# Optimization experiments

Measured on AMD Instinct MI355X. Metric: run time of the kernel, lower is better.

Reference implementation:

```python
import jax, jax.numpy as jnp
import numpy as np

K_V_DIM = 100
_SQRT_D = float(np.sqrt(K_V_DIM))


def _dk_layer(q, k, v, Wq, bq, Wk, n_unsqueeze):
    """One DKEncoder_layer: DK_text + DK_knowledge + DK_fusion (CokeBert attention).
    q: [B, q_dim]; k: [..., n, K_V_DIM]; v: [..., n, d_v].
    Attention over the last neighbor axis n.
    """
    # DK_text: linear + tanh + unsqueeze to broadcast against k
    q_i = jnp.tanh(q @ Wq.T + bq)                               # [B, D]
    q_i = q_i.reshape((q_i.shape[0],) + (1,) * n_unsqueeze + (K_V_DIM,))
    # DK_knowledge: bias-free linear on k
    k = k @ Wk.T
    # DK_fusion (CokeBert): scaled dot, mask zeros, leaky_relu+softmax, zero out fully-masked rows
    attn = (q_i * k).sum(-1) / _SQRT_D                          # [..., n]
    attn = jnp.where(attn == 0.0, -10000.0, attn)
    attn = jax.nn.softmax(jax.nn.leaky_relu(attn), axis=-1)
    n = attn.shape[-1]
    attn = jnp.where(attn == 1.0 / n, 0.0, attn)
    return jnp.einsum('...n,...nd->...d', attn, v)              # [..., d_v]


def setup_inputs() -> dict:
    key = jax.random.key(0)
    ks = jax.random.split(key, 12)
    B, S, E, N1, N2, D, Q = 8, 256, 256, 16, 16, K_V_DIM, 768
    return {
        "input_ent": jax.random.randint(ks[0], (B, S), 0, 2, dtype=jnp.int64),
        "q": jax.random.normal(ks[1], (B, S, Q), dtype=jnp.float32),
        "k1": jax.random.normal(ks[2], (B, E, N1, D), dtype=jnp.float32),
        "v1": jax.random.normal(ks[3], (B, E, N1, D), dtype=jnp.float32),
        "k2": jax.random.normal(ks[4], (B, E, N1, N2, D), dtype=jnp.float32),
        "v2": jax.random.normal(ks[5], (B, E, N1, N2, D), dtype=jnp.float32),
        # layers[0] has layer_no=2 (deepest), layers[1] has layer_no=1
        "Wq2": jax.random.normal(ks[6], (D, Q), dtype=jnp.float32) * 0.05,
        "bq2": jnp.zeros((D,), dtype=jnp.float32),
        "Wk2": jax.random.normal(ks[7], (D, D), dtype=jnp.float32) * 0.1,
        "Wq1": jax.random.normal(ks[8], (D, Q), dtype=jnp.float32) * 0.05,
        "bq1": jnp.zeros((D,), dtype=jnp.float32),
        "Wk1": jax.random.normal(ks[9], (D, D), dtype=jnp.float32) * 0.1,
    }


def reference(input_ent, q, k1, v1, k2, v2, Wq2, bq2, Wk2, Wq1, bq1, Wk1):
    q0 = q[:, 0, :]                                             # [B, Q]
    # layer 0 (layer_no=2): reduce innermost neighbor axis
    combined = _dk_layer(q0, k2, v2, Wq2, bq2, Wk2, 3)          # [B, E, N1, D]
    # layer 1 (layer_no=1): v = cat([v1, combined])
    v1c = jnp.concatenate([v1, combined], axis=-1)              # [B, E, N1, 2D]
    combined = _dk_layer(q0, k1, v1c, Wq1, bq1, Wk1, 2)         # [B, E, 2D]
    # scatter: i-th nonzero position of input_ent[b] receives combined[b, i]
    mask = input_ent != 0                                       # [B, S]
    rank = jnp.cumsum(mask.astype(jnp.int32), axis=1) - 1       # [B, S]
    rank = jnp.clip(rank, 0, combined.shape[1] - 1)
    gathered = jnp.take_along_axis(combined, rank[..., None], axis=1)  # [B, S, 2D]
    return jnp.where(mask[..., None], gathered, 0.0)
```

## Files before the change

### kernel.cpp

```cpp
#include <hip/hip_runtime.h>
#include <cstddef>
#include <cstdint>

#define BB 8
#define SS 256
#define EE 256
#define NN1 16
#define NN2 16
#define DD 100
#define QQ 768

__device__ __forceinline__ float dot4(float4 a, float4 b) {
    return a.x * b.x + a.y * b.y + a.z * b.z + a.w * b.w;
}

__global__ __launch_bounds__(256) void prep_kernel(
    const float* __restrict__ q, const int* __restrict__ ent,
    const float* __restrict__ Wq2, const float* __restrict__ bq2, const float* __restrict__ Wk2,
    const float* __restrict__ Wq1, const float* __restrict__ bq1, const float* __restrict__ Wk1,
    float* __restrict__ qk2o, float* __restrict__ qk1o, int* __restrict__ rk)
{
    const int blk = blockIdx.x, t = threadIdx.x;
    if (blk < 16) {
        const int b = blk >> 1, layer = blk & 1;
        const float* Wq = layer ? Wq1 : Wq2;
        const float* bq = layer ? bq1 : bq2;
        const float* Wk = layer ? Wk1 : Wk2;
        float* qko      = layer ? qk1o : qk2o;
        __shared__ float s_q[QQ];
        __shared__ float s_qi[DD];
        for (int i = t; i < QQ; i += 256) s_q[i] = q[(size_t)b * SS * QQ + i];
        __syncthreads();
        const float4* sq4 = (const float4*)s_q;
        const int r = t & 7;
        for (int d = t >> 3; d < DD; d += 32) {
            const float4* wq4 = (const float4*)(Wq + (size_t)d * QQ);
            float acc = 0.f;
            for (int c = r; c < QQ / 4; c += 8) acc += dot4(wq4[c], sq4[c]);
            acc += __shfl_xor(acc, 1, 8);
            acc += __shfl_xor(acc, 2, 8);
            acc += __shfl_xor(acc, 4, 8);
            if (r == 0) s_qi[d] = tanhf(acc + bq[d]);
        }
        __syncthreads();
        if (t < DD) {
            float acc = 0.f;
            for (int d = 0; d < DD; ++d) acc += s_qi[d] * Wk[d * DD + t];
            qko[b * DD + t] = 0.1f * acc;
        }
    } else {
        const int b = blk - 16;
        __shared__ int s_m[SS];
        const int m = (ent[b * SS + t] != 0) ? 1 : 0;
        s_m[t] = m;
        __syncthreads();
        for (int off = 1; off < SS; off <<= 1) {
            const int add = (t >= off) ? s_m[t - off] : 0;
            __syncthreads();
            s_m[t] += add;
            __syncthreads();
        }
        int rank = s_m[t] - 1;
        rank = rank < 0 ? 0 : (rank > EE - 1 ? EE - 1 : rank);
        rk[b * SS + t] = m ? rank : -1;
    }
}

__global__ __launch_bounds__(64) void dk2_kernel(
    const float* __restrict__ k2, const float* __restrict__ v2,
    const float* __restrict__ qk2g, float* __restrict__ c2o,
    int b0, int nunits)
{
    const int t = threadIdx.x;
    __shared__ float4 s_pp[400];
    float* s_part = (float*)s_pp;

    int u = blockIdx.x;
    const int stride = gridDim.x;
    const size_t gofs = (size_t)b0 * 4096;

    float4 ka[7];
    if (u < nunits) {
        const float4* kt = (const float4*)k2 + (gofs + u) * 400;
        #pragma unroll
        for (int j = 0; j < 6; ++j) ka[j] = kt[t + 64 * j];
        if (t < 16) ka[6] = kt[384 + t];
    }

    while (u < nunits) {
        const int b = b0 + (u >> 12);
        const float4* qk = (const float4*)qk2g + b * 25;
        const float4* vt = (const float4*)v2 + (gofs + u) * 400;

        float4 va[7];
        #pragma unroll
        for (int j = 0; j < 6; ++j) va[j] = vt[t + 64 * j];
        if (t < 16) va[6] = vt[384 + t];

        #pragma unroll
        for (int j = 0; j < 6; ++j) {
            const int i = t + 64 * j;
            s_part[i] = dot4(ka[j], qk[i % 25]);
        }
        if (t < 16) { const int i = 384 + t; s_part[i] = dot4(ka[6], qk[i % 25]); }

        const int un = u + stride;
        if (un < nunits) {
            const float4* ktn = (const float4*)k2 + (gofs + un) * 400;
            #pragma unroll
            for (int j = 0; j < 6; ++j) ka[j] = ktn[t + 64 * j];
            if (t < 16) ka[6] = ktn[384 + t];
        }

        __syncthreads();
        float p = 0.f;
        {
            float lg = 0.f;
            if (t < 16) {
                #pragma unroll
                for (int c = 0; c < 25; ++c) lg += s_part[t * 25 + c];
                if (lg == 0.0f) lg = -10000.0f;
                lg = lg >= 0.f ? lg : 0.01f * lg;
            }
            float mx = lg;
            mx = fmaxf(mx, __shfl_xor(mx, 1, 16));
            mx = fmaxf(mx, __shfl_xor(mx, 2, 16));
            mx = fmaxf(mx, __shfl_xor(mx, 4, 16));
            mx = fmaxf(mx, __shfl_xor(mx, 8, 16));
            const float e = __expf(lg - mx);
            float sm = e;
            sm += __shfl_xor(sm, 1, 16);
            sm += __shfl_xor(sm, 2, 16);
            sm += __shfl_xor(sm, 4, 16);
            sm += __shfl_xor(sm, 8, 16);
            p = e / sm;
            if (p == 0.0625f) p = 0.f;
        }
        __syncthreads();

        #pragma unroll
        for (int j = 0; j < 6; ++j) {
            const int i = t + 64 * j;
            const float pn = __shfl(p, i / 25, 64);
            s_pp[i] = make_float4(pn * va[j].x, pn * va[j].y, pn * va[j].z, pn * va[j].w);
        }
        if (t < 16) {
            const int i = 384 + t;
            const float pn = __shfl(p, 15, 64);
            s_pp[i] = make_float4(pn * va[6].x, pn * va[6].y, pn * va[6].z, pn * va[6].w);
        }
        __syncthreads();

        if (t < 25) {
            float4 a = make_float4(0.f, 0.f, 0.f, 0.f);
            #pragma unroll
            for (int n = 0; n < 16; ++n) {
                const float4 x = s_pp[n * 25 + t];
                a.x += x.x; a.y += x.y; a.z += x.z; a.w += x.w;
            }
            ((float4*)c2o)[(size_t)u * 25 + t] = a;
        }
        __syncthreads();
        u = un;
    }
}

__global__ __launch_bounds__(64) void dk1_kernel(
    const float* __restrict__ k1, const float* __restrict__ v1,
    const float* __restrict__ c2i, const float* __restrict__ qk1g,
    float* __restrict__ comb, int b0)
{
    const int blk  = blockIdx.x;
    const int bbe  = blk >> 1;
    const int half = blk & 1;
    const int b    = b0 + (bbe >> 8);
    const int be   = (b << 8) | (bbe & 255);
    const int t    = threadIdx.x;

    __shared__ float4 s_pp[400];
    float* s_part = (float*)s_pp;

    const float4* kt = (const float4*)k1 + (size_t)be * 400;
    const float4* vt = half ? (const float4*)c2i + (size_t)bbe * 400
                            : (const float4*)v1 + (size_t)be * 400;
    const float4* qk = (const float4*)qk1g + b * 25;

    float4 ka[7], va[7];
    #pragma unroll
    for (int j = 0; j < 6; ++j) { ka[j] = kt[t + 64 * j]; va[j] = vt[t + 64 * j]; }
    if (t < 16) { ka[6] = kt[384 + t]; va[6] = vt[384 + t]; }

    #pragma unroll
    for (int j = 0; j < 6; ++j) {
        const int i = t + 64 * j;
        s_part[i] = dot4(ka[j], qk[i % 25]);
    }
    if (t < 16) { const int i = 384 + t; s_part[i] = dot4(ka[6], qk[i % 25]); }
    __syncthreads();

    float p = 0.f;
    {
        float lg = 0.f;
        if (t < 16) {
            #pragma unroll
            for (int c = 0; c < 25; ++c) lg += s_part[t * 25 + c];
            if (lg == 0.0f) lg = -10000.0f;
            lg = lg >= 0.f ? lg : 0.01f * lg;
        }
        float mx = lg;
        mx = fmaxf(mx, __shfl_xor(mx, 1, 16));
        mx = fmaxf(mx, __shfl_xor(mx, 2, 16));
        mx = fmaxf(mx, __shfl_xor(mx, 4, 16));
        mx = fmaxf(mx, __shfl_xor(mx, 8, 16));
        const float e = __expf(lg - mx);
        float sm = e;
        sm += __shfl_xor(sm, 1, 16);
        sm += __shfl_xor(sm, 2, 16);
        sm += __shfl_xor(sm, 4, 16);
        sm += __shfl_xor(sm, 8, 16);
        p = e / sm;
        if (p == 0.0625f) p = 0.f;
    }
    __syncthreads();

    #pragma unroll
    for (int j = 0; j < 6; ++j) {
        const int i = t + 64 * j;
        const float pn = __shfl(p, i / 25, 64);
        s_pp[i] = make_float4(pn * va[j].x, pn * va[j].y, pn * va[j].z, pn * va[j].w);
    }
    if (t < 16) {
        const int i = 384 + t;
        const float pn = __shfl(p, 15, 64);
        s_pp[i] = make_float4(pn * va[6].x, pn * va[6].y, pn * va[6].z, pn * va[6].w);
    }
    __syncthreads();

    if (t < 25) {
        float4 a = make_float4(0.f, 0.f, 0.f, 0.f);
        #pragma unroll
        for (int n = 0; n < 16; ++n) {
            const float4 x = s_pp[n * 25 + t];
            a.x += x.x; a.y += x.y; a.z += x.z; a.w += x.w;
        }
        ((float4*)comb)[(size_t)be * 50 + half * 25 + t] = a;
    }
}

__global__ __launch_bounds__(64) void gather_kernel(
    const float* __restrict__ comb, const int* __restrict__ rk, float* __restrict__ out)
{
    const int bs = blockIdx.x;
    const int b  = bs >> 8;
    const int t  = threadIdx.x;
    const int r  = rk[bs];
    float* o = out + (size_t)bs * (2 * DD);
    if (r < 0) {
        for (int d = t; d < 2 * DD; d += 64) o[d] = 0.f;
    } else {
        const float* src = comb + (size_t)(b * EE + r) * (2 * DD);
        for (int d = t; d < 2 * DD; d += 64) o[d] = src[d];
    }
}

extern "C" void kernel_launch(void* const* d_in, const int* in_sizes, int n_in,
                              void* d_out, int out_size, void* d_ws, size_t ws_size,
                              hipStream_t stream)
{
    const int*   ent = (const int*)d_in[0];
    const float* q   = (const float*)d_in[1];
    const float* k1  = (const float*)d_in[2];
    const float* v1  = (const float*)d_in[3];
    const float* k2  = (const float*)d_in[4];
    const float* v2  = (const float*)d_in[5];
    const float* Wq2 = (const float*)d_in[6];
    const float* bq2 = (const float*)d_in[7];
    const float* Wk2 = (const float*)d_in[8];
    const float* Wq1 = (const float*)d_in[9];
    const float* bq1 = (const float*)d_in[10];
    const float* Wk1 = (const float*)d_in[11];
    float* out = (float*)d_out;

    float* ws   = (float*)d_ws;
    float* qk2  = ws;
    float* qk1  = ws + 1024;
    int*   rk   = (int*)(ws + 2048);
    float* comb = ws + 4096;
    float* c2   = ws + 4096 + 409600;

    const size_t fixed = 4096 + 409600;
    const size_t perb  = (size_t)EE * NN1 * DD;
    size_t wsf = ws_size / sizeof(float);
    int kb = (wsf > fixed) ? (int)((wsf - fixed) / perb) : 1;
    if (kb < 1) kb = 1;
    if (kb > BB) kb = BB;

    prep_kernel<<<24, 256, 0, stream>>>(q, ent, Wq2, bq2, Wk2, Wq1, bq1, Wk1, qk2, qk1, rk);
    for (int b0 = 0; b0 < BB; b0 += kb) {
        const int nb = (BB - b0 < kb) ? (BB - b0) : kb;
        const int nunits = nb * EE * NN1;
        const int grid = nunits < 4096 ? nunits : 4096;
        dk2_kernel<<<grid, 64, 0, stream>>>(k2, v2, qk2, c2, b0, nunits);
        dk1_kernel<<<nb * EE * 2, 64, 0, stream>>>(k1, v1, c2, qk1, comb, b0);
    }
    gather_kernel<<<BB * SS, 64, 0, stream>>>(comb, rk, out);
}
```

Before: 155.0 us.

## Batch four units per dk2 block with staged loads and shared qk cache

Each dk2 block now processes four (b,e,n1) units per iteration. It issues all four k tiles and then the v tiles up front so more memory traffic is in flight, replacing the single-unit software prefetch. The qk vectors are cached in shared memory once per block, and the grid size is changed to match. This raises register pressure (56 float4 per thread) and LDS use, which may lower occupancy. The loop also assumes nunits is a multiple of four and that a group of four never crosses a batch boundary.

```diff
diff --git a/kernel.cpp b/kernel.cpp
--- a/kernel.cpp
+++ b/kernel.cpp
@@ -69,99 +69,83 @@
 __global__ __launch_bounds__(64) void dk2_kernel(
     const float* __restrict__ k2, const float* __restrict__ v2,
     const float* __restrict__ qk2g, float* __restrict__ c2o,
-    int b0, int nunits)
+    int b0, int nb, int nunits)
 {
     const int t = threadIdx.x;
+    __shared__ float  s_part[1600];
     __shared__ float4 s_pp[400];
-    float* s_part = (float*)s_pp;
-
-    int u = blockIdx.x;
-    const int stride = gridDim.x;
-    const size_t gofs = (size_t)b0 * 4096;
-
-    float4 ka[7];
-    if (u < nunits) {
-        const float4* kt = (const float4*)k2 + (gofs + u) * 400;
-        #pragma unroll
-        for (int j = 0; j < 6; ++j) ka[j] = kt[t + 64 * j];
-        if (t < 16) ka[6] = kt[384 + t];
-    }
-
-    while (u < nunits) {
-        const int b = b0 + (u >> 12);
-        const float4* qk = (const float4*)qk2g + b * 25;
-        const float4* vt = (const float4*)v2 + (gofs + u) * 400;
-
-        float4 va[7];
-        #pragma unroll
-        for (int j = 0; j < 6; ++j) va[j] = vt[t + 64 * j];
-        if (t < 16) va[6] = vt[384 + t];
-
-        #pragma unroll
-        for (int j = 0; j < 6; ++j) {
-            const int i = t + 64 * j;
-            s_part[i] = dot4(ka[j], qk[i % 25]);
-        }
-        if (t < 16) { const int i = 384 + t; s_part[i] = dot4(ka[6], qk[i % 25]); }
-
-        const int un = u + stride;
-        if (un < nunits) {
-            const float4* ktn = (const float4*)k2 + (gofs + un) * 400;
-            #pragma unroll
-            for (int j = 0; j < 6; ++j) ka[j] = ktn[t + 64 * j];
-            if (t < 16) ka[6] = ktn[384 + t];
-        }
-
-        __syncthreads();
-        float p = 0.f;
-        {
-            float lg = 0.f;
-            if (t < 16) {
-                #pragma unroll
-                for (int c = 0; c < 25; ++c) lg += s_part[t * 25 + c];
-                if (lg == 0.0f) lg = -10000.0f;
-                lg = lg >= 0.f ? lg : 0.01f * lg;
-            }
-            float mx = lg;
-            mx = fmaxf(mx, __shfl_xor(mx, 1, 16));
-            mx = fmaxf(mx, __shfl_xor(mx, 2, 16));
-            mx = fmaxf(mx, __shfl_xor(mx, 4, 16));
-            mx = fmaxf(mx, __shfl_xor(mx, 8, 16));
-            const float e = __expf(lg - mx);
-            float sm = e;
-            sm += __shfl_xor(sm, 1, 16);
-            sm += __shfl_xor(sm, 2, 16);
-            sm += __shfl_xor(sm, 4, 16);
-            sm += __shfl_xor(sm, 8, 16);
-            p = e / sm;
-            if (p == 0.0625f) p = 0.f;
-        }
-        __syncthreads();
-
-        #pragma unroll
-        for (int j = 0; j < 6; ++j) {
-            const int i = t + 64 * j;
-            const float pn = __shfl(p, i / 25, 64);
-            s_pp[i] = make_float4(pn * va[j].x, pn * va[j].y, pn * va[j].z, pn * va[j].w);
-        }
-        if (t < 16) {
-            const int i = 384 + t;
-            const float pn = __shfl(p, 15, 64);
-            s_pp[i] = make_float4(pn * va[6].x, pn * va[6].y, pn * va[6].z, pn * va[6].w);
-        }
-        __syncthreads();
-
-        if (t < 25) {
-            float4 a = make_float4(0.f, 0.f, 0.f, 0.f);
-            #pragma unroll
-            for (int n = 0; n < 16; ++n) {
-                const float4 x = s_pp[n * 25 + t];
-                a.x += x.x; a.y += x.y; a.z += x.z; a.w += x.w;
-            }
-            ((float4*)c2o)[(size_t)u * 25 + t] = a;
-        }
-        __syncthreads();
-        u = un;
+    __shared__ float  s_qk[800];
+
+    for (int i = t; i < nb * DD; i += 64) s_qk[i] = qk2g[b0 * DD + i];
+    __syncthreads();
+    const float4* sqk = (const float4*)s_qk;
+
+    for (int u0 = blockIdx.x * 4; u0 < nunits; u0 += gridDim.x * 4) {
+        const int brel = u0 >> 12;
+        const float4* qk = sqk + brel * 25;
+        const float4* kt = (const float4*)k2 + ((size_t)b0 * 4096 + u0) * 400;
+        const float4* vt = (const float4*)v2 + ((size_t)b0 * 4096 + u0) * 400;
+
+        float4 ka0[7], ka1[7], ka2[7], ka3[7];
+        float4 va0[7], va1[7], va2[7], va3[7];
+        float p0, p1, p2, p3;
+
+#define LDX(A, PTR, base)                                                     \
+        { _Pragma("unroll") for (int j = 0; j < 6; ++j) A[j] = (PTR)[(base) + t + 64*j]; \
+          if (t < 16) A[6] = (PTR)[(base) + 384 + t]; }
+
+#define DOTS(A, po)                                                           \
+        { _Pragma("unroll") for (int j = 0; j < 6; ++j) { const int i = t + 64*j; \
+              s_part[(po) + i] = dot4(A[j], qk[i % 25]); }                    \
+          if (t < 16) { const int i = 384 + t; s_part[(po) + i] = dot4(A[6], qk[i % 25]); } }
+
+#define SMAX(P, po)                                                           \
+        { float lg = 0.f;                                                     \
+          if (t < 16) {                                                       \
+              _Pragma("unroll") for (int c = 0; c < 25; ++c) lg += s_part[(po) + t * 25 + c]; \
+              if (lg == 0.0f) lg = -10000.0f;                                 \
+              lg = lg >= 0.f ? lg : 0.01f * lg;                               \
+          }                                                                   \
+          float mx = lg;                                                      \
+          mx = fmaxf(mx, __shfl_xor(mx, 1, 16));                              \
+          mx = fmaxf(mx, __shfl_xor(mx, 2, 16));                              \
+          mx = fmaxf(mx, __shfl_xor(mx, 4, 16));                              \
+          mx = fmaxf(mx, __shfl_xor(mx, 8, 16));                              \
+          const float e = __expf(lg - mx);                                    \
+          float sm = e;                                                       \
+          sm += __shfl_xor(sm, 1, 16);                                        \
+          sm += __shfl_xor(sm, 2, 16);                                        \
+          sm += __shfl_xor(sm, 4, 16);                                        \
+          sm += __shfl_xor(sm, 8, 16);                                        \
+          P = e / sm;                                                         \
+          if (P == 0.0625f) P = 0.f; }
+
+#define PV(A, P, uu)                                                          \
+        { _Pragma("unroll") for (int j = 0; j < 6; ++j) { const int i = t + 64*j; \
+              const float pn = __shfl(P, i / 25, 64);                         \
+              s_pp[i] = make_float4(pn*A[j].x, pn*A[j].y, pn*A[j].z, pn*A[j].w); } \
+          if (t < 16) { const int i = 384 + t;                                \
+              const float pn = __shfl(P, 15, 64);                             \
+              s_pp[i] = make_float4(pn*A[6].x, pn*A[6].y, pn*A[6].z, pn*A[6].w); } \
+          __syncthreads();                                                    \
+          if (t < 25) { float4 a = make_float4(0.f,0.f,0.f,0.f);              \
+              _Pragma("unroll") for (int n = 0; n < 16; ++n) {                \
+                  const float4 x = s_pp[n * 25 + t];                          \
+                  a.x += x.x; a.y += x.y; a.z += x.z; a.w += x.w; }           \
+              ((float4*)c2o)[(size_t)(uu) * 25 + t] = a; }                    \
+          __syncthreads(); }
+
+        LDX(ka0, kt, 0) LDX(ka1, kt, 400) LDX(ka2, kt, 800) LDX(ka3, kt, 1200)
+        DOTS(ka0, 0)     LDX(va0, vt, 0)     SMAX(p0, 0)
+        DOTS(ka1, 400)   LDX(va1, vt, 400)   SMAX(p1, 400)
+        DOTS(ka2, 800)   LDX(va2, vt, 800)   SMAX(p2, 800)
+        DOTS(ka3, 1200)  LDX(va3, vt, 1200)  SMAX(p3, 1200)
+        PV(va0, p0, u0) PV(va1, p1, u0 + 1) PV(va2, p2, u0 + 2) PV(va3, p3, u0 + 3)
+
+#undef LDX
+#undef DOTS
+#undef SMAX
+#undef PV
     }
 }
 
@@ -299,8 +283,9 @@
     for (int b0 = 0; b0 < BB; b0 += kb) {
         const int nb = (BB - b0 < kb) ? (BB - b0) : kb;
         const int nunits = nb * EE * NN1;
-        const int grid = nunits < 4096 ? nunits : 4096;
-        dk2_kernel<<<grid, 64, 0, stream>>>(k2, v2, qk2, c2, b0, nunits);
+        int grid = (nunits + 3) / 4;
+        if (grid > 3072) grid = 3072;
+        dk2_kernel<<<grid, 64, 0, stream>>>(k2, v2, qk2, c2, b0, nb, nunits);
         dk1_kernel<<<nb * EE * 2, 64, 0, stream>>>(k1, v1, c2, qk1, comb, b0);
     }
     gather_kernel<<<BB * SS, 64, 0, stream>>>(comb, rk, out);
```

After: 155.4 us. Within noise of the previous version (+0.2%).
